# Performance work log

Hardware: AMD Instinct MI355X
Metric: run time of the kernel (lower is better)

The kernel has to match this reference:

```python
import jax, jax.numpy as jnp
import numpy as np

D_MODEL = 512
D_DOWN = 64          # q and k each have this width; downsample outputs 2*D_DOWN
DIST_BINS = 64
ANGLE_BINS = 36
D_HID = DIST_BINS + ANGLE_BINS  # MLP hidden and output width (100)


def setup_inputs() -> dict:
    key = jax.random.key(0)
    ks = jax.random.split(key, 7)
    B, N = 2, 512
    s_down = 1.0 / np.sqrt(D_MODEL)
    s1 = 1.0 / np.sqrt(2 * D_DOWN)
    s2 = 1.0 / np.sqrt(D_HID)
    return {
        "x": jax.random.normal(ks[0], (B, N, D_MODEL), dtype=jnp.float32),
        "W_down": jax.random.uniform(ks[1], (D_MODEL, 2 * D_DOWN), jnp.float32, -s_down, s_down),
        "b_down": jax.random.uniform(ks[2], (2 * D_DOWN,), jnp.float32, -s_down, s_down),
        "W1": jax.random.uniform(ks[3], (2 * D_DOWN, D_HID), jnp.float32, -s1, s1),
        "b1": jax.random.uniform(ks[4], (D_HID,), jnp.float32, -s1, s1),
        "W2": jax.random.uniform(ks[5], (D_HID, D_HID), jnp.float32, -s2, s2),
        "b2": jax.random.uniform(ks[6], (D_HID,), jnp.float32, -s2, s2),
    }


def reference(x, W_down, b_down, W1, b1, W2, b2):
    # downsample: [B,N,d_model] -> [B,N,2*d_down], split into q,k of d_down each
    qk = x @ W_down + b_down
    q, k = jnp.split(qk, 2, axis=-1)              # each [B,N,d_down]
    q_i = q[:, :, None, :]                        # [B,N,1,d]
    k_j = k[:, None, :, :]                        # [B,1,N,d]
    pw = jnp.concatenate([q_i * k_j, k_j - q_i], axis=-1)  # [B,N,N,2*d_down]
    h = jax.nn.silu(pw @ W1 + b1)                 # [B,N,N,D_HID]
    out = h @ W2 + b2                             # [B,N,N,D_HID]
    distogram = out[..., :DIST_BINS]
    anglogram = out[..., DIST_BINS:]
    return (distogram, anglogram)
```

## Files before the change

### kernel.cpp

```cpp
#include <hip/hip_runtime.h>
#include <hip/hip_bf16.h>
#include <cstdint>

#define NBATCH 2
#define NSEQ   512
#define DHID   100

typedef __bf16 bf16x8 __attribute__((ext_vector_type(8)));
typedef float  f32x4  __attribute__((ext_vector_type(4)));

__global__ __launch_bounds__(128)
void proj_kernel(const float* __restrict__ x, const float* __restrict__ Wd,
                 const float* __restrict__ bd, float* __restrict__ qk)
{
    __shared__ float xs[512];
    const int row = blockIdx.x;
    const int tid = threadIdx.x;
    const float* xr = x + row * 512;
    #pragma unroll
    for (int e = 0; e < 4; e++) xs[tid + 128 * e] = xr[tid + 128 * e];
    __syncthreads();
    float acc = bd[tid];
    #pragma unroll 8
    for (int e = 0; e < 512; e++)
        acc = fmaf(xs[e], Wd[e * 128 + tid], acc);
    qk[row * 128 + tid] = acc;
}


#define LDS_W2T  28672
#define LDS_H    57344
#define LDS_TOT  122880

__global__ __launch_bounds__(512, 2)
void pair_mlp_kernel(const float* __restrict__ qk,
                     const float* __restrict__ W1, const float* __restrict__ b1,
                     const float* __restrict__ W2, const float* __restrict__ b2,
                     float* __restrict__ dist, float* __restrict__ ang)
{
    extern __shared__ char smem[];
    const int tid  = threadIdx.x;
    const int w    = tid >> 6;
    const int lane = tid & 63;
    const int l16  = lane & 15;
    const int g    = lane >> 4;

    for (int idx = tid; idx < LDS_TOT / 4; idx += 512)
        ((float*)smem)[idx] = 0.f;
    __syncthreads();

    for (int idx = tid; idx < 100 * 128; idx += 512) {
        int n = idx >> 7, k = idx & 127;
        int byte = n * 256 + ((2 * k) ^ ((n & 7) << 4));
        *(__bf16*)(smem + byte) = (__bf16)W1[k * DHID + n];
    }
    for (int idx = tid; idx < 100 * 100; idx += 512) {
        int n = idx / 100, k = idx % 100;
        int byte = LDS_W2T + n * 256 + ((2 * k) ^ ((n & 7) << 4));
        *(__bf16*)(smem + byte) = (__bf16)W2[k * DHID + n];
    }
    __syncthreads();

    float b1v[7], b2v[7];
    #pragma unroll
    for (int nt = 0; nt < 7; nt++) {
        int n = nt * 16 + l16;
        b1v[nt] = (n < DHID) ? b1[n] : 0.f;
        b2v[nt] = (n < DHID) ? b2[n] : 0.f;
    }

    char* hb = smem + LDS_H + w * 8192;
    const int TILES = NBATCH * (NSEQ / 8) * (NSEQ / 32);

    for (int t = blockIdx.x; t < TILES; t += gridDim.x) {
        int tmp = t;
        const int jb = tmp & 15;  tmp >>= 4;
        const int ib = tmp & 63;  tmp >>= 6;
        const int bi = tmp;
        const int i  = ib * 8 + w;
        const int j0 = jb * 32;

        const float* qrow = qk + (size_t)(bi * NSEQ + i) * 128;
        f32x4 qa0 = *(const f32x4*)(qrow + g * 8);
        f32x4 qa1 = *(const f32x4*)(qrow + g * 8 + 4);
        f32x4 qb0 = *(const f32x4*)(qrow + 32 + g * 8);
        f32x4 qb1 = *(const f32x4*)(qrow + 32 + g * 8 + 4);

        bf16x8 af[2][4];
        #pragma unroll
        for (int s = 0; s < 2; s++) {
            const float* krow = qk + (size_t)(bi * NSEQ + j0 + s * 16 + l16) * 128 + 64;
            f32x4 ka0 = *(const f32x4*)(krow + g * 8);
            f32x4 ka1 = *(const f32x4*)(krow + g * 8 + 4);
            f32x4 kb0 = *(const f32x4*)(krow + 32 + g * 8);
            f32x4 kb1 = *(const f32x4*)(krow + 32 + g * 8 + 4);
            #pragma unroll
            for (int j = 0; j < 4; j++) {
                af[s][0][j]     = (__bf16)(qa0[j] * ka0[j]);
                af[s][0][j + 4] = (__bf16)(qa1[j] * ka1[j]);
                af[s][1][j]     = (__bf16)(qb0[j] * kb0[j]);
                af[s][1][j + 4] = (__bf16)(qb1[j] * kb1[j]);
                af[s][2][j]     = (__bf16)(ka0[j] - qa0[j]);
                af[s][2][j + 4] = (__bf16)(ka1[j] - qa1[j]);
                af[s][3][j]     = (__bf16)(kb0[j] - qb0[j]);
                af[s][3][j + 4] = (__bf16)(kb1[j] - qb1[j]);
            }
        }

        f32x4 acc1[2][7];
        #pragma unroll
        for (int nt = 0; nt < 7; nt++) {
            f32x4 init = {b1v[nt], b1v[nt], b1v[nt], b1v[nt]};
            acc1[0][nt] = init; acc1[1][nt] = init;
        }
        #pragma unroll
        for (int nt = 0; nt < 7; nt++) {
            const int rbase = (nt * 16 + l16) * 256;
            const int sw    = ((nt * 16 + l16) & 7) << 4;
            #pragma unroll
            for (int ks = 0; ks < 4; ks++) {
                bf16x8 bf = *(const bf16x8*)(smem + rbase + ((64 * ks + 16 * g) ^ sw));
                acc1[0][nt] = __builtin_amdgcn_mfma_f32_16x16x32_bf16(af[0][ks], bf, acc1[0][nt], 0, 0, 0);
                acc1[1][nt] = __builtin_amdgcn_mfma_f32_16x16x32_bf16(af[1][ks], bf, acc1[1][nt], 0, 0, 0);
            }
        }

        #pragma unroll
        for (int s = 0; s < 2; s++)
            #pragma unroll
            for (int nt = 0; nt < 7; nt++)
                #pragma unroll
                for (int r = 0; r < 4; r++) {
                    float z  = acc1[s][nt][r];
                    float hv = z / (1.f + __expf(-z));
                    if (nt == 6 && l16 >= 4) hv = 0.f;
                    int rr   = s * 16 + g * 4 + r;
                    int col  = nt * 16 + l16;
                    int byte = rr * 256 + ((2 * col) ^ ((rr & 7) << 4));
                    *(__bf16*)(hb + byte) = (__bf16)hv;
                }

        f32x4 acc2[2][7];
        #pragma unroll
        for (int nt = 0; nt < 7; nt++) {
            f32x4 init = {b2v[nt], b2v[nt], b2v[nt], b2v[nt]};
            acc2[0][nt] = init; acc2[1][nt] = init;
        }
        #pragma unroll
        for (int ks = 0; ks < 4; ks++) {
            bf16x8 ah[2];
            #pragma unroll
            for (int s = 0; s < 2; s++) {
                int row = s * 16 + l16;
                ah[s] = *(const bf16x8*)(hb + row * 256 + ((64 * ks + 16 * g) ^ ((row & 7) << 4)));
            }
            #pragma unroll
            for (int nt = 0; nt < 7; nt++) {
                int row = nt * 16 + l16;
                bf16x8 bf = *(const bf16x8*)(smem + LDS_W2T + row * 256 + ((64 * ks + 16 * g) ^ ((row & 7) << 4)));
                acc2[0][nt] = __builtin_amdgcn_mfma_f32_16x16x32_bf16(ah[0], bf, acc2[0][nt], 0, 0, 0);
                acc2[1][nt] = __builtin_amdgcn_mfma_f32_16x16x32_bf16(ah[1], bf, acc2[1][nt], 0, 0, 0);
            }
        }

        const size_t rowbase = (size_t)(bi * NSEQ + i) * NSEQ + j0;
        #pragma unroll
        for (int s = 0; s < 2; s++)
            #pragma unroll
            for (int r = 0; r < 4; r++) {
                size_t prow = rowbase + s * 16 + g * 4 + r;
                float* dptr = dist + prow * 64;
                float* aptr = ang  + prow * 36;
                #pragma unroll
                for (int nt = 0; nt < 7; nt++) {
                    float v = acc2[s][nt][r];
                    int n = nt * 16 + l16;
                    if (n < 64)            dptr[n] = v;
                    else if (n < DHID)     aptr[n - 64] = v;
                }
            }
    }
}

extern "C" void kernel_launch(void* const* d_in, const int* in_sizes, int n_in,
                              void* d_out, int out_size, void* d_ws, size_t ws_size,
                              hipStream_t stream) {
    const float* x  = (const float*)d_in[0];
    const float* Wd = (const float*)d_in[1];
    const float* bd = (const float*)d_in[2];
    const float* W1 = (const float*)d_in[3];
    const float* b1 = (const float*)d_in[4];
    const float* W2 = (const float*)d_in[5];
    const float* b2 = (const float*)d_in[6];

    float* dist = (float*)d_out;
    float* ang  = dist + (size_t)NBATCH * NSEQ * NSEQ * 64;
    float* qk   = (float*)d_ws;

    (void)hipFuncSetAttribute(reinterpret_cast<const void*>(&pair_mlp_kernel),
                              hipFuncAttributeMaxDynamicSharedMemorySize, LDS_TOT);

    proj_kernel<<<NBATCH * NSEQ, 128, 0, stream>>>(x, Wd, bd, qk);
    pair_mlp_kernel<<<256, 512, LDS_TOT, stream>>>(qk, W1, b1, W2, b2, dist, ang);
}
```

Measured before the change: 279.2 us.

## Transpose MFMA operands for vectorized hidden and output stores, split proj accumulators

Swaps the A/B operands of both MFMA stages so each lane holds four consecutive output columns for one pair row. The SiLU result can then go to LDS as one bf16x4 store, and the final results as f32x4 vector global stores instead of scalar stores. Bias loading is vectorized, the divide becomes a hardware reciprocal, and the projection kernel uses four independent accumulators. The transposed fragment layout and the swizzle indexing must match exactly, and the approximate reciprocal slightly changes numerics.

```diff
diff --git a/kernel.cpp b/kernel.cpp
--- a/kernel.cpp
+++ b/kernel.cpp
@@ -7,6 +7,7 @@
 #define DHID   100
 
 typedef __bf16 bf16x8 __attribute__((ext_vector_type(8)));
+typedef __bf16 bf16x4 __attribute__((ext_vector_type(4)));
 typedef float  f32x4  __attribute__((ext_vector_type(4)));
 
 __global__ __launch_bounds__(128)
@@ -20,11 +21,16 @@
     #pragma unroll
     for (int e = 0; e < 4; e++) xs[tid + 128 * e] = xr[tid + 128 * e];
     __syncthreads();
-    float acc = bd[tid];
-    #pragma unroll 8
-    for (int e = 0; e < 512; e++)
-        acc = fmaf(xs[e], Wd[e * 128 + tid], acc);
-    qk[row * 128 + tid] = acc;
+    float a0 = 0.f, a1 = 0.f, a2 = 0.f, a3 = 0.f;
+    const float* wp = Wd + tid;
+    #pragma unroll 4
+    for (int e = 0; e < 512; e += 4) {
+        a0 = fmaf(xs[e],     wp[(e)     * 128], a0);
+        a1 = fmaf(xs[e + 1], wp[(e + 1) * 128], a1);
+        a2 = fmaf(xs[e + 2], wp[(e + 2) * 128], a2);
+        a3 = fmaf(xs[e + 3], wp[(e + 3) * 128], a3);
+    }
+    qk[row * 128 + tid] = bd[tid] + ((a0 + a1) + (a2 + a3));
 }
 
 
@@ -44,6 +50,7 @@
     const int lane = tid & 63;
     const int l16  = lane & 15;
     const int g    = lane >> 4;
+    const int swz  = (l16 & 7) << 4;
 
     for (int idx = tid; idx < LDS_TOT / 4; idx += 512)
         ((float*)smem)[idx] = 0.f;
@@ -61,12 +68,12 @@
     }
     __syncthreads();
 
-    float b1v[7], b2v[7];
+    f32x4 b1v[7], b2v[7];
     #pragma unroll
     for (int nt = 0; nt < 7; nt++) {
-        int n = nt * 16 + l16;
-        b1v[nt] = (n < DHID) ? b1[n] : 0.f;
-        b2v[nt] = (n < DHID) ? b2[n] : 0.f;
+        int n0 = nt * 16 + g * 4;
+        if (n0 + 3 < DHID) { b1v[nt] = *(const f32x4*)(b1 + n0); b2v[nt] = *(const f32x4*)(b2 + n0); }
+        else               { b1v[nt] = (f32x4){0,0,0,0};         b2v[nt] = (f32x4){0,0,0,0}; }
     }
 
     char* hb = smem + LDS_H + w * 8192;
@@ -109,76 +116,65 @@
 
         f32x4 acc1[2][7];
         #pragma unroll
-        for (int nt = 0; nt < 7; nt++) {
-            f32x4 init = {b1v[nt], b1v[nt], b1v[nt], b1v[nt]};
-            acc1[0][nt] = init; acc1[1][nt] = init;
-        }
+        for (int nt = 0; nt < 7; nt++) { acc1[0][nt] = b1v[nt]; acc1[1][nt] = b1v[nt]; }
         #pragma unroll
         for (int nt = 0; nt < 7; nt++) {
             const int rbase = (nt * 16 + l16) * 256;
-            const int sw    = ((nt * 16 + l16) & 7) << 4;
             #pragma unroll
             for (int ks = 0; ks < 4; ks++) {
-                bf16x8 bf = *(const bf16x8*)(smem + rbase + ((64 * ks + 16 * g) ^ sw));
-                acc1[0][nt] = __builtin_amdgcn_mfma_f32_16x16x32_bf16(af[0][ks], bf, acc1[0][nt], 0, 0, 0);
-                acc1[1][nt] = __builtin_amdgcn_mfma_f32_16x16x32_bf16(af[1][ks], bf, acc1[1][nt], 0, 0, 0);
-            }
-        }
-
-        #pragma unroll
-        for (int s = 0; s < 2; s++)
-            #pragma unroll
-            for (int nt = 0; nt < 7; nt++)
+                bf16x8 wf = *(const bf16x8*)(smem + rbase + ((64 * ks + 16 * g) ^ swz));
+                acc1[0][nt] = __builtin_amdgcn_mfma_f32_16x16x32_bf16(wf, af[0][ks], acc1[0][nt], 0, 0, 0);
+                acc1[1][nt] = __builtin_amdgcn_mfma_f32_16x16x32_bf16(wf, af[1][ks], acc1[1][nt], 0, 0, 0);
+            }
+        }
+
+        #pragma unroll
+        for (int s = 0; s < 2; s++) {
+            char* hrow = hb + (s * 16 + l16) * 256;
+            #pragma unroll
+            for (int nt = 0; nt < 7; nt++) {
+                bf16x4 hv;
                 #pragma unroll
                 for (int r = 0; r < 4; r++) {
-                    float z  = acc1[s][nt][r];
-                    float hv = z / (1.f + __expf(-z));
-                    if (nt == 6 && l16 >= 4) hv = 0.f;
-                    int rr   = s * 16 + g * 4 + r;
-                    int col  = nt * 16 + l16;
-                    int byte = rr * 256 + ((2 * col) ^ ((rr & 7) << 4));
-                    *(__bf16*)(hb + byte) = (__bf16)hv;
+                    float z = acc1[s][nt][r];
+                    float v = z * __builtin_amdgcn_rcpf(1.f + __expf(-z));
+                    if (nt == 6 && g > 0) v = 0.f;
+                    hv[r] = (__bf16)v;
                 }
+                *(bf16x4*)(hrow + ((nt * 32 + g * 8) ^ swz)) = hv;
+            }
+        }
 
         f32x4 acc2[2][7];
         #pragma unroll
-        for (int nt = 0; nt < 7; nt++) {
-            f32x4 init = {b2v[nt], b2v[nt], b2v[nt], b2v[nt]};
-            acc2[0][nt] = init; acc2[1][nt] = init;
-        }
+        for (int nt = 0; nt < 7; nt++) { acc2[0][nt] = b2v[nt]; acc2[1][nt] = b2v[nt]; }
         #pragma unroll
         for (int ks = 0; ks < 4; ks++) {
             bf16x8 ah[2];
             #pragma unroll
-            for (int s = 0; s < 2; s++) {
-                int row = s * 16 + l16;
-                ah[s] = *(const bf16x8*)(hb + row * 256 + ((64 * ks + 16 * g) ^ ((row & 7) << 4)));
-            }
+            for (int s = 0; s < 2; s++)
+                ah[s] = *(const bf16x8*)(hb + (s * 16 + l16) * 256 + ((ks * 64 + g * 16) ^ swz));
             #pragma unroll
             for (int nt = 0; nt < 7; nt++) {
-                int row = nt * 16 + l16;
-                bf16x8 bf = *(const bf16x8*)(smem + LDS_W2T + row * 256 + ((64 * ks + 16 * g) ^ ((row & 7) << 4)));
-                acc2[0][nt] = __builtin_amdgcn_mfma_f32_16x16x32_bf16(ah[0], bf, acc2[0][nt], 0, 0, 0);
-                acc2[1][nt] = __builtin_amdgcn_mfma_f32_16x16x32_bf16(ah[1], bf, acc2[1][nt], 0, 0, 0);
+                bf16x8 wf = *(const bf16x8*)(smem + LDS_W2T + (nt * 16 + l16) * 256 + ((ks * 64 + 16 * g) ^ swz));
+                acc2[0][nt] = __builtin_amdgcn_mfma_f32_16x16x32_bf16(wf, ah[0], acc2[0][nt], 0, 0, 0);
+                acc2[1][nt] = __builtin_amdgcn_mfma_f32_16x16x32_bf16(wf, ah[1], acc2[1][nt], 0, 0, 0);
             }
         }
 
         const size_t rowbase = (size_t)(bi * NSEQ + i) * NSEQ + j0;
         #pragma unroll
-        for (int s = 0; s < 2; s++)
-            #pragma unroll
-            for (int r = 0; r < 4; r++) {
-                size_t prow = rowbase + s * 16 + g * 4 + r;
-                float* dptr = dist + prow * 64;
-                float* aptr = ang  + prow * 36;
-                #pragma unroll
-                for (int nt = 0; nt < 7; nt++) {
-                    float v = acc2[s][nt][r];
-                    int n = nt * 16 + l16;
-                    if (n < 64)            dptr[n] = v;
-                    else if (n < DHID)     aptr[n - 64] = v;
-                }
-            }
+        for (int s = 0; s < 2; s++) {
+            size_t prow = rowbase + s * 16 + l16;
+            float* dp = dist + prow * 64;
+            float* ap = ang  + prow * 36;
+            #pragma unroll
+            for (int nt = 0; nt < 4; nt++)
+                *(f32x4*)(dp + nt * 16 + g * 4) = acc2[s][nt];
+            *(f32x4*)(ap + g * 4)      = acc2[s][4];
+            *(f32x4*)(ap + 16 + g * 4) = acc2[s][5];
+            if (g == 0) *(f32x4*)(ap + 32) = acc2[s][6];
+        }
     }
 }
 
```

Result: faster. 250.8 us (-10.2%).
